# Optimization experiments

Hardware: AMD Instinct MI355X
Metric: run time of the kernel (lower is better)

The kernel has to match this reference:

```python
import jax, jax.numpy as jnp
from jax import lax
import numpy as np

DN = ('NCHW', 'OIHW', 'NCHW')


def conv3x3(x, w, b):
    y = lax.conv_general_dilated(x, w, (1, 1), ((1, 1), (1, 1)), dimension_numbers=DN)
    return y + b[None, :, None, None]


def box_mean(x, k):
    # Uniform k x k box mean with reflect padding; separable (exactly equal to
    # the dense ones/k^2 conv in the original since the kernel is rank-1).
    pad = k // 2
    C = x.shape[1]
    xp = jnp.pad(x, ((0, 0), (0, 0), (pad, pad), (pad, pad)), mode='reflect')
    kh = jnp.ones((C, 1, k, 1), x.dtype) / k
    kw = jnp.ones((C, 1, 1, k), x.dtype) / k
    y = lax.conv_general_dilated(xp, kh, (1, 1), 'VALID', feature_group_count=C, dimension_numbers=DN)
    y = lax.conv_general_dilated(y, kw, (1, 1), 'VALID', feature_group_count=C, dimension_numbers=DN)
    return y


def std_map_for_window(features, k):
    # features: [N, 8, H, W]
    C = features.shape[1]
    m = box_mean(features, k)
    m2 = box_mean(features * features, k)
    var = jnp.maximum(m2 - m * m, 1e-6)
    w = jax.nn.softmax(jnp.ones((C,), features.dtype))  # uniform (C==8 branch)
    sm = jnp.einsum('nchw,c->nhw', jnp.sqrt(var), w)[:, None]  # [N,1,H,W]
    return jnp.power(sm, 0.8)


def setup_inputs() -> dict:
    key = jax.random.key(0)
    ks = jax.random.split(key, 8)
    B, H, W = 8, 512, 512
    x = jax.random.normal(ks[0], (B, 4, H, W), dtype=jnp.float32)
    s = 0.05
    conv1_w = jax.random.normal(ks[1], (32, 4, 3, 3), jnp.float32) * s
    conv1_b = jnp.zeros((32,), jnp.float32)
    conv2_w = jax.random.normal(ks[2], (16, 32, 3, 3), jnp.float32) * s
    conv2_b = jnp.zeros((16,), jnp.float32)
    conv3_w = jax.random.normal(ks[3], (8, 16, 3, 3), jnp.float32) * s
    conv3_b = jnp.zeros((8,), jnp.float32)
    fusion_w = jnp.full((1, 3, 1, 1), 1.0 / 3.0, jnp.float32)  # init per module
    fusion_b = jnp.zeros((1,), jnp.float32)
    channel_weights = jnp.ones((4,), jnp.float32) / 4.0
    return dict(x=x, conv1_w=conv1_w, conv1_b=conv1_b, conv2_w=conv2_w,
                conv2_b=conv2_b, conv3_w=conv3_w, conv3_b=conv3_b,
                fusion_w=fusion_w, fusion_b=fusion_b,
                channel_weights=channel_weights)


def reference(x, conv1_w, conv1_b, conv2_w, conv2_b, conv3_w, conv3_b,
              fusion_w, fusion_b, channel_weights):
    window_sizes = (11, 25, 49)
    # feature extractor
    f = jax.nn.leaky_relu(conv3x3(x, conv1_w, conv1_b), 0.2)
    f = jax.nn.leaky_relu(conv3x3(f, conv2_w, conv2_b), 0.2)
    f = conv3x3(f, conv3_w, conv3_b)  # [B,8,H,W]
    # multi-scale std maps
    maps = [std_map_for_window(f, k) for k in window_sizes]
    multi = jnp.concatenate(maps, axis=1)  # [B,3,H,W]
    fused = jax.nn.relu(
        lax.conv_general_dilated(multi, fusion_w, (1, 1), 'VALID', dimension_numbers=DN)
        + fusion_b[None, :, None, None])  # [B,1,H,W]
    # adaptive thresholds
    std_flat = fused.ravel()
    q = jnp.quantile(std_flat, jnp.array([0.25, 0.75], fused.dtype))
    q25, q75 = q[0], q[1]
    iqr = q75 - q25
    iqr = jnp.where(iqr < 1e-5, jnp.asarray(0.05, fused.dtype), iqr)
    global_std = jnp.std(x, axis=(2, 3), keepdims=True, ddof=1)  # [B,4,1,1]
    lower = jnp.broadcast_to((q25 - 0.5 * iqr), global_std.shape)
    upper = jnp.broadcast_to((q75 + 0.5 * iqr), global_std.shape)
    gf = jnp.clip(global_std * 5.0, 0.5, 2.0)
    lower = lower * gf
    upper = upper * gf
    cw = jax.nn.softmax(channel_weights).reshape(1, 4, 1, 1)
    channel_std = jnp.std(x * cw, axis=(2, 3), keepdims=True, ddof=1)
    cf = jnp.clip(channel_std * 2.0, 0.8, 1.2)
    lower = lower * cf
    upper = upper * cf
    degenerate = jnp.min(jnp.abs(upper - lower)) < 1e-5
    mean_t = (upper + lower) / 2
    lower = jnp.where(degenerate, mean_t - 0.05, lower)
    upper = jnp.where(degenerate, mean_t + 0.05, upper)
    # texture mask
    diff = jnp.maximum(upper - lower, 1e-5)
    norm = jnp.clip((fused - lower) / diff, 0.0, 1.0)  # [B,4,H,W] via broadcast
    mask = jax.nn.sigmoid(6.0 * norm - 3.0)
    return jnp.mean(mask, axis=1, keepdims=True)  # [B,1,H,W]
```

## Files before the change

kernel.cpp:

```cpp
#include <hip/hip_runtime.h>
#include <hip/hip_bf16.h>
#include <math.h>


__global__ __launch_bounds__(256, 2) void conv12_k(
    const float* __restrict__ x,
    const float* __restrict__ w1,
    const float* __restrict__ b1,
    const float* __restrict__ w2,
    const float* __restrict__ b2,
    float* __restrict__ f2)
{
    __shared__ float xs[4 * 36 * 68];
    __shared__ float f1s[4 * 34 * 68];

    const int t  = threadIdx.x;
    const int tx = t & 7;
    const int ty = t >> 3;
    const int x0 = blockIdx.x * 64;
    const int y0 = blockIdx.y * 32;
    const int bb = blockIdx.z;
    const float* xb = x + (size_t)bb * 4 * 262144;

    for (int i = t; i < 9792; i += 256) {
        int ci  = i / 2448;
        int rem = i - ci * 2448;
        int r   = rem / 68;
        int c   = rem - r * 68;
        int Y = y0 - 2 + r, X = x0 - 2 + c;
        float v = 0.f;
        if ((unsigned)Y < 512u && (unsigned)X < 512u)
            v = xb[ci * 262144 + Y * 512 + X];
        xs[i] = v;
    }

    float acc[16][8];
#pragma unroll
    for (int j = 0; j < 16; ++j)
#pragma unroll
        for (int p = 0; p < 8; ++p) acc[j][p] = 0.f;

    for (int g = 0; g < 8; ++g) {
        __syncthreads();

#pragma unroll
        for (int fc = 0; fc < 4; ++fc) {
            const int foc = g * 4 + fc;
            float wv[36];
#pragma unroll
            for (int k = 0; k < 36; ++k) wv[k] = w1[foc * 36 + k];
            const float bias = b1[foc];
            for (int it = t; it < 578; it += 256) {
                int r  = it / 17;
                int q  = it - r * 17;
                int c0 = q * 4;
                int Y1 = y0 - 1 + r;
                float v[4] = {bias, bias, bias, bias};
#pragma unroll
                for (int ci = 0; ci < 4; ++ci) {
#pragma unroll
                    for (int ky = 0; ky < 3; ++ky) {
                        const float* xr = &xs[ci * 2448 + (r + ky) * 68 + c0];
                        float4 a  = *(const float4*)xr;
                        float2 bl = *(const float2*)(xr + 4);
                        float rr[6] = {a.x, a.y, a.z, a.w, bl.x, bl.y};
#pragma unroll
                        for (int kx = 0; kx < 3; ++kx) {
                            float w = wv[ci * 9 + ky * 3 + kx];
#pragma unroll
                            for (int p = 0; p < 4; ++p)
                                v[p] = fmaf(rr[p + kx], w, v[p]);
                        }
                    }
                }
                float st[4];
                bool rowok = ((unsigned)Y1 < 512u);
#pragma unroll
                for (int p = 0; p < 4; ++p) {
                    int X1 = x0 - 1 + c0 + p;
                    bool ok = rowok && ((unsigned)X1 < 512u) && (c0 + p <= 65);
                    float tv = v[p];
                    tv = tv > 0.f ? tv : 0.2f * tv;
                    st[p] = ok ? tv : 0.f;
                }
                *(float4*)&f1s[fc * 2312 + r * 68 + c0] =
                    make_float4(st[0], st[1], st[2], st[3]);
            }
        }
        __syncthreads();

#pragma unroll
        for (int fc = 0; fc < 4; ++fc) {
            const int ci = g * 4 + fc;
#pragma unroll
            for (int dy = 0; dy < 3; ++dy) {
                const float* rowp = &f1s[fc * 2312 + (ty + dy) * 68 + tx * 8];
                float4 a0 = *(const float4*)(rowp);
                float4 a1 = *(const float4*)(rowp + 4);
                float2 a2 = *(const float2*)(rowp + 8);
                float rr[10] = {a0.x, a0.y, a0.z, a0.w,
                                a1.x, a1.y, a1.z, a1.w, a2.x, a2.y};
#pragma unroll
                for (int j = 0; j < 16; ++j) {
#pragma unroll
                    for (int dx = 0; dx < 3; ++dx) {
                        float w = w2[(j * 32 + ci) * 9 + dy * 3 + dx];
#pragma unroll
                        for (int p = 0; p < 8; ++p)
                            acc[j][p] = fmaf(rr[p + dx], w, acc[j][p]);
                    }
                }
            }
        }
    }

    const int y = y0 + ty;
#pragma unroll
    for (int j = 0; j < 16; ++j) {
        float b = b2[j];
        float* op = f2 + (((size_t)bb * 16 + j) * 512 + y) * 512 + x0 + tx * 8;
        float v[8];
#pragma unroll
        for (int p = 0; p < 8; ++p) {
            float tv = acc[j][p] + b;
            v[p] = tv > 0.f ? tv : 0.2f * tv;
        }
        ((float4*)op)[0] = make_float4(v[0], v[1], v[2], v[3]);
        ((float4*)op)[1] = make_float4(v[4], v[5], v[6], v[7]);
    }
}

__global__ __launch_bounds__(256) void conv3_k(
    const float* __restrict__ in,
    const float* __restrict__ wgt,
    const float* __restrict__ bias,
    float* __restrict__ out)
{
    constexpr int TW = 64, TH = 32, SW = TW + 4;
    __shared__ float sl[(TH + 2) * SW];

    const int tx = threadIdx.x & 7;
    const int ty = threadIdx.x >> 3;
    const int x0 = blockIdx.x * TW;
    const int y0 = blockIdx.y * TH;
    const int bb = blockIdx.z;

    const float* inb = in + (size_t)bb * 16 * 262144;

    float acc[8][8];
#pragma unroll
    for (int j = 0; j < 8; ++j)
#pragma unroll
        for (int p = 0; p < 8; ++p) acc[j][p] = 0.f;

    for (int ci = 0; ci < 16; ++ci) {
        __syncthreads();
        const float* ip = inb + (size_t)ci * 262144;
        for (int idx = threadIdx.x; idx < (TH + 2) * (TW + 2); idx += 256) {
            int r  = idx / (TW + 2);
            int cc = idx - r * (TW + 2);
            int yy = y0 - 1 + r, xx = x0 - 1 + cc;
            float v = 0.f;
            if ((unsigned)yy < 512u && (unsigned)xx < 512u) v = ip[yy * 512 + xx];
            sl[r * SW + cc] = v;
        }
        __syncthreads();
        const float* wci = wgt + (size_t)ci * 9;
#pragma unroll
        for (int dy = 0; dy < 3; ++dy) {
            const float* rowp = &sl[(ty + dy) * SW + tx * 8];
            float4 a0 = *(const float4*)(rowp);
            float4 a1 = *(const float4*)(rowp + 4);
            float2 a2 = *(const float2*)(rowp + 8);
            float rr[10] = {a0.x, a0.y, a0.z, a0.w,
                            a1.x, a1.y, a1.z, a1.w, a2.x, a2.y};
#pragma unroll
            for (int j = 0; j < 8; ++j) {
#pragma unroll
                for (int dx = 0; dx < 3; ++dx) {
                    float w = wci[(size_t)j * 16 * 9 + dy * 3 + dx];
#pragma unroll
                    for (int p = 0; p < 8; ++p)
                        acc[j][p] = fmaf(rr[p + dx], w, acc[j][p]);
                }
            }
        }
    }

    const int y = y0 + ty;
#pragma unroll
    for (int j = 0; j < 8; ++j) {
        float b = bias[j];
        float* op = out + (((size_t)bb * 8 + j) * 512 + y) * 512 + x0 + tx * 8;
        float v[8];
#pragma unroll
        for (int p = 0; p < 8; ++p) v[p] = acc[j][p] + b;
        ((float4*)op)[0] = make_float4(v[0], v[1], v[2], v[3]);
        ((float4*)op)[1] = make_float4(v[4], v[5], v[6], v[7]);
    }
}

__device__ __forceinline__ float2 f2add(float2 a, float2 b) {
    return make_float2(a.x + b.x, a.y + b.y);
}
__device__ __forceinline__ int mir(int v) {
    return v < 0 ? -v : (v > 511 ? 1022 - v : v);
}

#define YB 4

__global__ __launch_bounds__(256) void stdmap_k(
    const float* __restrict__ f,
    const float* __restrict__ fw,
    const float* __restrict__ fbp,
    float* __restrict__ fused,
    int b0)
{
    const int total = gridDim.x * gridDim.y;
    const int lin   = blockIdx.y * gridDim.x + blockIdx.x;
    const int task  = (lin & 7) * (total >> 3) + (lin >> 3);
    const int bb    = task >> 7;
    const int y0    = (task & 127) * YB;
    const int t    = threadIdx.x;
    const int lane = t & 63, wid = t >> 6;

    __shared__ float S[3][2][513];
    __shared__ float wtt[4][6];

    const int   RAD[3] = {5, 12, 24};
    const float INV[3] = {1.f/121.f, 1.f/625.f, 1.f/2401.f};

    float smacc[3][YB][2];
#pragma unroll
    for (int sc = 0; sc < 3; ++sc)
#pragma unroll
        for (int yy = 0; yy < YB; ++yy)
            { smacc[sc][yy][0] = 0.f; smacc[sc][yy][1] = 0.f; }

    for (int c = 0; c < 8; ++c) {
        const float* base = f + ((size_t)bb * 8 + c) * 512 * 512;

        float2 wf[3], wq[3];
        {
            float2 sf[3] = {{0.f,0.f},{0.f,0.f},{0.f,0.f}};
            float2 sq[3] = {{0.f,0.f},{0.f,0.f},{0.f,0.f}};
#pragma unroll
            for (int dy = -24; dy <= 24; ++dy) {
                int row = mir(y0 + dy);
                float2 v  = ((const float2*)(base + (size_t)row * 512))[t];
                float2 vq = make_float2(v.x * v.x, v.y * v.y);
                int ad = dy < 0 ? -dy : dy;
                int ring = ad <= 5 ? 0 : (ad <= 12 ? 1 : 2);
                sf[ring] = f2add(sf[ring], v);
                sq[ring] = f2add(sq[ring], vq);
            }
            wf[0] = sf[0];               wq[0] = sq[0];
            wf[1] = f2add(sf[1], wf[0]); wq[1] = f2add(sq[1], wq[0]);
            wf[2] = f2add(sf[2], wf[1]); wq[2] = f2add(sq[2], wq[1]);
        }

        for (int yy = 0; yy < YB; ++yy) {
            const int y = y0 + yy;
            if (yy > 0) {
#pragma unroll
                for (int sc = 0; sc < 3; ++sc) {
                    int ra = mir(y + RAD[sc]);
                    int rs = mir(y - 1 - RAD[sc]);
                    float2 va = ((const float2*)(base + (size_t)ra * 512))[t];
                    float2 vs = ((const float2*)(base + (size_t)rs * 512))[t];
                    wf[sc].x += va.x - vs.x;       wf[sc].y += va.y - vs.y;
                    wq[sc].x += va.x*va.x - vs.x*vs.x;
                    wq[sc].y += va.y*va.y - vs.y*vs.y;
                }
            }

            float pf[3], pq[3], incf[3], incq[3];
#pragma unroll
            for (int sc = 0; sc < 3; ++sc) {
                pf[sc] = wf[sc].x + wf[sc].y;
                pq[sc] = wq[sc].x + wq[sc].y;
                incf[sc] = pf[sc]; incq[sc] = pq[sc];
            }
#pragma unroll
            for (int off = 1; off < 64; off <<= 1) {
#pragma unroll
                for (int sc = 0; sc < 3; ++sc) {
                    float uf = __shfl_up(incf[sc], (unsigned)off, 64);
                    float uq = __shfl_up(incq[sc], (unsigned)off, 64);
                    if (lane >= off) { incf[sc] += uf; incq[sc] += uq; }
                }
            }
            if (lane == 63) {
#pragma unroll
                for (int sc = 0; sc < 3; ++sc) {
                    wtt[wid][sc]     = incf[sc];
                    wtt[wid][3 + sc] = incq[sc];
                }
            }
            __syncthreads();
            float wpf[3] = {0.f,0.f,0.f}, wpq[3] = {0.f,0.f,0.f};
#pragma unroll
            for (int w = 0; w < 4; ++w)
                if (w < wid)
#pragma unroll
                    for (int sc = 0; sc < 3; ++sc) {
                        wpf[sc] += wtt[w][sc];
                        wpq[sc] += wtt[w][3 + sc];
                    }
#pragma unroll
            for (int sc = 0; sc < 3; ++sc) {
                float exf = wpf[sc] + incf[sc] - pf[sc];
                float exq = wpq[sc] + incq[sc] - pq[sc];
                S[sc][0][2*t+1] = exf + wf[sc].x;
                S[sc][0][2*t+2] = exf + pf[sc];
                S[sc][1][2*t+1] = exq + wq[sc].x;
                S[sc][1][2*t+2] = exq + pq[sc];
            }
            if (t == 0)
#pragma unroll
                for (int sc = 0; sc < 3; ++sc)
                    { S[sc][0][0] = 0.f; S[sc][1][0] = 0.f; }
            __syncthreads();

#pragma unroll
            for (int sc = 0; sc < 3; ++sc) {
                const int r = RAD[sc];
                const float* Sf = S[sc][0];
                const float* Sq = S[sc][1];
#pragma unroll
                for (int slot = 0; slot < 2; ++slot) {
                    int xx = 2*t + slot;
                    int lo = xx - r, hi = xx + r;
                    int loc = lo < 0 ? 0 : lo;
                    int hic = hi > 511 ? 511 : hi;
                    float wfv = Sf[hic + 1] - Sf[loc];
                    float wqv = Sq[hic + 1] - Sq[loc];
                    if (lo < 0)   { wfv += Sf[r - xx + 1] - Sf[1];
                                    wqv += Sq[r - xx + 1] - Sq[1]; }
                    if (hi > 511) { wfv += Sf[511] - Sf[1022 - xx - r];
                                    wqv += Sq[511] - Sq[1022 - xx - r]; }
                    float m   = wfv * INV[sc];
                    float m2  = wqv * INV[sc];
                    float var = m2 - m * m;
                    var = var > 1e-6f ? var : 1e-6f;
                    smacc[sc][yy][slot] += sqrtf(var);
                }
            }
            __syncthreads();
        }
    }

    const float w0 = fw[0], w1 = fw[1], w2 = fw[2], b = fbp[0];
#pragma unroll
    for (int yy = 0; yy < YB; ++yy) {
        float o[2];
#pragma unroll
        for (int slot = 0; slot < 2; ++slot) {
            float m0 = powf(smacc[0][yy][slot] * 0.125f, 0.8f);
            float m1 = powf(smacc[1][yy][slot] * 0.125f, 0.8f);
            float m2 = powf(smacc[2][yy][slot] * 0.125f, 0.8f);
            float fv = w0 * m0 + w1 * m1 + w2 * m2 + b;
            o[slot] = fv > 0.f ? fv : 0.f;
        }
        ((float2*)(fused + ((size_t)(b0 + bb) * 512 + y0 + yy) * 512))[t] =
            make_float2(o[0], o[1]);
    }
}

__global__ __launch_bounds__(256) void plane_std_part_k(
    const float* __restrict__ x, double* __restrict__ part)
{
    const int plane = blockIdx.x >> 5;
    const int blk   = blockIdx.x & 31;
    const float* p = x + (size_t)plane * 262144 + (size_t)blk * 8192;
    double s = 0.0, s2 = 0.0;
    for (int i = threadIdx.x; i < 2048; i += 256) {
        float4 v = ((const float4*)p)[i];
        s  += (double)v.x + (double)v.y + (double)v.z + (double)v.w;
        s2 += (double)v.x * v.x + (double)v.y * v.y
            + (double)v.z * v.z + (double)v.w * v.w;
    }
    __shared__ double ls[256], ls2[256];
    ls[threadIdx.x] = s; ls2[threadIdx.x] = s2;
    __syncthreads();
    for (int off = 128; off > 0; off >>= 1) {
        if (threadIdx.x < off) {
            ls[threadIdx.x]  += ls[threadIdx.x + off];
            ls2[threadIdx.x] += ls2[threadIdx.x + off];
        }
        __syncthreads();
    }
    if (threadIdx.x == 0) {
        part[2 * blockIdx.x]     = ls[0];
        part[2 * blockIdx.x + 1] = ls2[0];
    }
}

__global__ void plane_std_fin_k(const double* __restrict__ part,
                                float* __restrict__ stds)
{
    const int plane = threadIdx.x;
    if (plane >= 32) return;
    double s = 0.0, s2 = 0.0;
    for (int b = 0; b < 32; ++b) {
        s  += part[2 * (plane * 32 + b)];
        s2 += part[2 * (plane * 32 + b) + 1];
    }
    const double N = 262144.0;
    double var = (s2 - s * s / N) / (N - 1.0);
    stds[plane] = (float)sqrt(var > 0.0 ? var : 0.0);
}

__global__ __launch_bounds__(256) void hist1_k(
    const float* __restrict__ fused, unsigned* __restrict__ h)
{
    __shared__ unsigned lh[4096];
    for (int i = threadIdx.x; i < 4096; i += 256) lh[i] = 0u;
    __syncthreads();
    const int base = blockIdx.x * 2048;
    for (int i = threadIdx.x; i < 2048; i += 256) {
        unsigned bits = __float_as_uint(fused[base + i]);
        atomicAdd(&lh[bits >> 20], 1u);
    }
    __syncthreads();
    for (int i = threadIdx.x; i < 4096; i += 256) {
        unsigned c = lh[i];
        if (c) atomicAdd(&h[i], c);
    }
}

__global__ __launch_bounds__(256) void select_par_k(
    const unsigned* __restrict__ h, unsigned* __restrict__ pfx,
    unsigned* __restrict__ rem, int level)
{
    const int tt = blockIdx.x;
    const int t = threadIdx.x, lane = t & 63, wid = t >> 6;
    const unsigned targets[4] = {524287u, 524288u, 1572863u, 1572864u};
    const unsigned R = (level == 1) ? targets[tt] : rem[tt];
    const unsigned* hb = (level == 1) ? h : h + tt * 4096;

    unsigned loc[16], lsum = 0;
    const uint4* hv = (const uint4*)(hb + t * 16);
#pragma unroll
    for (int i = 0; i < 4; ++i) {
        uint4 v = hv[i];
        loc[4*i]=v.x; loc[4*i+1]=v.y; loc[4*i+2]=v.z; loc[4*i+3]=v.w;
        lsum += v.x + v.y + v.z + v.w;
    }
    __shared__ unsigned warr[4];
    __shared__ unsigned rbin, rrem;
    unsigned inc = lsum;
#pragma unroll
    for (int off = 1; off < 64; off <<= 1) {
        unsigned up = __shfl_up(inc, (unsigned)off, 64);
        if (lane >= off) inc += up;
    }
    if (lane == 63) warr[wid] = inc;
    __syncthreads();
    unsigned wpre = 0;
#pragma unroll
    for (int w = 0; w < 4; ++w) if (w < wid) wpre += warr[w];
    unsigned ex = wpre + inc - lsum;
    if (R >= ex && R < ex + lsum) {
        unsigned cum = ex;
#pragma unroll
        for (int i = 0; i < 16; ++i) {
            if (cum + loc[i] > R) { rbin = (unsigned)(t * 16 + i); rrem = R - cum; break; }
            cum += loc[i];
        }
    }
    __syncthreads();
    if (t == 0) {
        if (level == 1) { pfx[tt] = rbin << 20; rem[tt] = rrem; }
        else            { pfx[tt] |= rbin << 8; rem[tt] = rrem; }
    }
}

__global__ __launch_bounds__(256) void hist2_k(
    const float* __restrict__ fused, const unsigned* __restrict__ pfx,
    unsigned* __restrict__ h2)
{
    __shared__ unsigned lh[4 * 4096];
    for (int i = threadIdx.x; i < 4 * 4096; i += 256) lh[i] = 0u;
    unsigned p0 = pfx[0] >> 20, p1 = pfx[1] >> 20,
             p2 = pfx[2] >> 20, p3 = pfx[3] >> 20;
    __syncthreads();
    const int base = blockIdx.x * 2048;
    for (int i = threadIdx.x; i < 2048; i += 256) {
        unsigned bits = __float_as_uint(fused[base + i]);
        unsigned top = bits >> 20;
        unsigned mid = (bits >> 8) & 0xFFFu;
        if (top == p0) atomicAdd(&lh[0 * 4096 + mid], 1u);
        if (top == p1) atomicAdd(&lh[1 * 4096 + mid], 1u);
        if (top == p2) atomicAdd(&lh[2 * 4096 + mid], 1u);
        if (top == p3) atomicAdd(&lh[3 * 4096 + mid], 1u);
    }
    __syncthreads();
    for (int i = threadIdx.x; i < 4 * 4096; i += 256) {
        unsigned c = lh[i];
        if (c) atomicAdd(&h2[i], c);
    }
}

__global__ __launch_bounds__(256) void hist3_k(
    const float* __restrict__ fused, const unsigned* __restrict__ pfx,
    unsigned* __restrict__ h3)
{
    __shared__ unsigned lh[4 * 256];
    for (int i = threadIdx.x; i < 4 * 256; i += 256) lh[i] = 0u;
    unsigned p0 = pfx[0] >> 8, p1 = pfx[1] >> 8,
             p2 = pfx[2] >> 8, p3 = pfx[3] >> 8;
    __syncthreads();
    const int base = blockIdx.x * 2048;
    for (int i = threadIdx.x; i < 2048; i += 256) {
        unsigned bits = __float_as_uint(fused[base + i]);
        unsigned top = bits >> 8;
        unsigned low = bits & 0xFFu;
        if (top == p0) atomicAdd(&lh[0 * 256 + low], 1u);
        if (top == p1) atomicAdd(&lh[1 * 256 + low], 1u);
        if (top == p2) atomicAdd(&lh[2 * 256 + low], 1u);
        if (top == p3) atomicAdd(&lh[3 * 256 + low], 1u);
    }
    __syncthreads();
    for (int i = threadIdx.x; i < 4 * 256; i += 256) {
        unsigned c = lh[i];
        if (c) atomicAdd(&h3[i], c);
    }
}

__device__ __forceinline__ float clampf(float v, float lo, float hi) {
    return v < lo ? lo : (v > hi ? hi : v);
}

__global__ __launch_bounds__(256) void finalize_k(
    const unsigned* __restrict__ h3,
    const unsigned* __restrict__ pfx,
    const unsigned* __restrict__ rem,
    const float* __restrict__ stds,
    const float* __restrict__ cw,
    float* __restrict__ lu)
{
    const int tt = threadIdx.x >> 6, lane = threadIdx.x & 63;
    __shared__ float vals[4];

    {
        const unsigned R = rem[tt];
        const unsigned* h = h3 + tt * 256;
        uint4 v = ((const uint4*)h)[lane];
        unsigned loc[4] = {v.x, v.y, v.z, v.w};
        unsigned lsum = v.x + v.y + v.z + v.w;
        unsigned inc = lsum;
#pragma unroll
        for (int off = 1; off < 64; off <<= 1) {
            unsigned up = __shfl_up(inc, (unsigned)off, 64);
            if (lane >= off) inc += up;
        }
        unsigned ex = inc - lsum;
        if (R >= ex && R < ex + lsum) {
            unsigned cum = ex;
#pragma unroll
            for (int i = 0; i < 4; ++i) {
                if (cum + loc[i] > R) {
                    vals[tt] = __uint_as_float(pfx[tt] | (unsigned)(lane * 4 + i));
                    break;
                }
                cum += loc[i];
            }
        }
    }
    __syncthreads();
    if (threadIdx.x != 0) return;

    float q25 = vals[0] + 0.75f * (vals[1] - vals[0]);
    float q75 = vals[2] + 0.25f * (vals[3] - vals[2]);
    float iqr = q75 - q25;
    if (iqr < 1e-5f) iqr = 0.05f;
    float lo0 = q25 - 0.5f * iqr, up0 = q75 + 0.5f * iqr;

    float mx = cw[0];
    for (int c = 1; c < 4; ++c) mx = cw[c] > mx ? cw[c] : mx;
    float e[4], se = 0.f;
    for (int c = 0; c < 4; ++c) { e[c] = expf(cw[c] - mx); se += e[c]; }

    float l[32], u[32], mind = 1e30f;
    for (int p = 0; p < 32; ++p) {
        float sd = stds[p];
        int c = p & 3;
        float gf = clampf(sd * 5.f, 0.5f, 2.f);
        float cf = clampf(sd * (e[c] / se) * 2.f, 0.8f, 1.2f);
        l[p] = lo0 * gf * cf;
        u[p] = up0 * gf * cf;
        float d = fabsf(u[p] - l[p]);
        if (d < mind) mind = d;
    }
    bool deg = mind < 1e-5f;
    for (int p = 0; p < 32; ++p) {
        float L = l[p], U = u[p];
        if (deg) { float m = 0.5f * (L + U); L = m - 0.05f; U = m + 0.05f; }
        lu[p] = L; lu[32 + p] = U;
    }
}

__global__ __launch_bounds__(256) void mask_k(
    const float* __restrict__ fused, const float* __restrict__ lu,
    float* __restrict__ out)
{
    const int b = blockIdx.y;
    const int i = blockIdx.x * 256 + threadIdx.x;
    float fv = fused[(size_t)b * 262144 + i];
    float s = 0.f;
#pragma unroll
    for (int c = 0; c < 4; ++c) {
        float L = lu[b * 4 + c], U = lu[32 + b * 4 + c];
        float d = U - L; d = d > 1e-5f ? d : 1e-5f;
        float n = (fv - L) / d;
        n = n < 0.f ? 0.f : (n > 1.f ? 1.f : n);
        s += 1.f / (1.f + expf(3.f - 6.f * n));
    }
    out[(size_t)b * 262144 + i] = 0.25f * s;
}

extern "C" void kernel_launch(void* const* d_in, const int* in_sizes, int n_in,
                              void* d_out, int out_size, void* d_ws, size_t ws_size,
                              hipStream_t stream)
{
    const float* x   = (const float*)d_in[0];
    const float* c1w = (const float*)d_in[1];
    const float* c1b = (const float*)d_in[2];
    const float* c2w = (const float*)d_in[3];
    const float* c2b = (const float*)d_in[4];
    const float* c3w = (const float*)d_in[5];
    const float* c3b = (const float*)d_in[6];
    const float* fw  = (const float*)d_in[7];
    const float* fb  = (const float*)d_in[8];
    const float* cwt = (const float*)d_in[9];
    float* out = (float*)d_out;
    char* ws = (char*)d_ws;

    const size_t PLANE = 512 * 512;

    float* fused = (float*)ws;
    size_t off = 8 * PLANE * sizeof(float);
    float* stds = (float*)(ws + off); off += 32 * 4;
    float* lu   = (float*)(ws + off); off += 64 * 4;
    off = (off + 255) & ~(size_t)255;
    unsigned* pfx = (unsigned*)(ws + off); off += 16;
    unsigned* rem = (unsigned*)(ws + off); off += 16;
    off = (off + 255) & ~(size_t)255;
    unsigned* h1 = (unsigned*)(ws + off); off += 4096 * 4;
    unsigned* h2 = (unsigned*)(ws + off); off += 4 * 4096 * 4;
    unsigned* h3 = (unsigned*)(ws + off); off += 4 * 256 * 4;
    off = (off + 255) & ~(size_t)255;
    double* part = (double*)(ws + off); off += 1024 * 2 * sizeof(double);
    off = (off + 1023) & ~(size_t)1023;

    const size_t perb = 24 * PLANE * sizeof(float);
    int nb = 8;
    while (nb > 1 && off + (size_t)nb * perb > ws_size) nb >>= 1;
    float* f2  = (float*)(ws + off);
    float* fch = f2 + (size_t)nb * 16 * PLANE;

    hipLaunchKernelGGL(plane_std_part_k, dim3(1024), dim3(256), 0, stream, x, part);
    hipLaunchKernelGGL(plane_std_fin_k,  dim3(1),    dim3(64),  0, stream, part, stds);

    for (int b0 = 0; b0 < 8; b0 += nb) {
        const float* xc = x + (size_t)b0 * 4 * PLANE;
        hipLaunchKernelGGL(conv12_k, dim3(8, 16, nb), dim3(256), 0, stream,
                           xc, c1w, c1b, c2w, c2b, f2);
        hipLaunchKernelGGL(conv3_k,  dim3(8, 16, nb), dim3(256), 0, stream,
                           f2, c3w, c3b, fch);
        hipLaunchKernelGGL(stdmap_k, dim3(512 / YB, nb), dim3(256), 0, stream,
                           fch, fw, fb, fused, b0);
    }

    hipMemsetAsync(h1, 0, (4096 + 4 * 4096 + 4 * 256) * 4, stream);
    hipLaunchKernelGGL(hist1_k,     dim3(1024), dim3(256), 0, stream, fused, h1);
    hipLaunchKernelGGL(select_par_k, dim3(4),   dim3(256), 0, stream, h1, pfx, rem, 1);
    hipLaunchKernelGGL(hist2_k,     dim3(1024), dim3(256), 0, stream, fused, pfx, h2);
    hipLaunchKernelGGL(select_par_k, dim3(4),   dim3(256), 0, stream, h2, pfx, rem, 2);
    hipLaunchKernelGGL(hist3_k,     dim3(1024), dim3(256), 0, stream, fused, pfx, h3);
    hipLaunchKernelGGL(finalize_k,  dim3(1),    dim3(256), 0, stream,
                       h3, pfx, rem, stds, cwt, lu);
    hipLaunchKernelGGL(mask_k, dim3(1024, 8), dim3(256), 0, stream, fused, lu, out);
}
```

Baseline: 1.114 ms.

## Restructure fused conv1+conv2 kernel as row-streaming rolling buffer

```diff
diff --git a/kernel.cpp b/kernel.cpp
--- a/kernel.cpp
+++ b/kernel.cpp
@@ -3,7 +3,7 @@
 #include <math.h>
 
 
-__global__ __launch_bounds__(256, 2) void conv12_k(
+__global__ __launch_bounds__(256, 3) void conv12_k(
     const float* __restrict__ x,
     const float* __restrict__ w1,
     const float* __restrict__ b1,
@@ -11,122 +11,157 @@
     const float* __restrict__ b2,
     float* __restrict__ f2)
 {
-    __shared__ float xs[4 * 36 * 68];
-    __shared__ float f1s[4 * 34 * 68];
+    __shared__ float xr[3][4][68];
+    __shared__ float f1r[3][32][68];
+    __shared__ float w2s[32 * 16 * 12];
 
     const int t  = threadIdx.x;
-    const int tx = t & 7;
-    const int ty = t >> 3;
     const int x0 = blockIdx.x * 64;
     const int y0 = blockIdx.y * 32;
     const int bb = blockIdx.z;
     const float* xb = x + (size_t)bb * 4 * 262144;
 
-    for (int i = t; i < 9792; i += 256) {
-        int ci  = i / 2448;
-        int rem = i - ci * 2448;
-        int r   = rem / 68;
-        int c   = rem - r * 68;
-        int Y = y0 - 2 + r, X = x0 - 2 + c;
-        float v = 0.f;
-        if ((unsigned)Y < 512u && (unsigned)X < 512u)
-            v = xb[ci * 262144 + Y * 512 + X];
-        xs[i] = v;
-    }
-
-    float acc[16][8];
-#pragma unroll
-    for (int j = 0; j < 16; ++j)
-#pragma unroll
-        for (int p = 0; p < 8; ++p) acc[j][p] = 0.f;
-
-    for (int g = 0; g < 8; ++g) {
+    for (int i = t; i < 4608; i += 256) {
+        int kk = i % 9;
+        int r  = i / 9;
+        int j  = r & 15, ci = r >> 4;
+        w2s[(ci * 16 + j) * 12 + kk] = w2[(j * 32 + ci) * 9 + kk];
+    }
+
+    const int foc = t >> 3, oc = t & 7;
+    const int j2  = t >> 4, cg = t & 15;
+    float wv[36];
+#pragma unroll
+    for (int k = 0; k < 36; ++k) wv[k] = w1[foc * 36 + k];
+    const float f1b = b1[foc];
+    const float b2v = b2[j2];
+
+    auto stage_x = [&](int Y) {
+        const int slot = (unsigned)(Y + 516) % 3u;
+        for (int i = t; i < 272; i += 256) {
+            int ci = i / 68, c = i - ci * 68;
+            int X = x0 - 2 + c;
+            float v = 0.f;
+            if ((unsigned)Y < 512u && (unsigned)X < 512u)
+                v = xb[ci * 262144 + Y * 512 + X];
+            xr[slot][ci][c] = v;
+        }
+    };
+
+    auto f1_row = [&](int Y1) {
+        const int sw = (unsigned)(Y1 + 516) % 3u;
+        int sk[3];
+#pragma unroll
+        for (int ky = 0; ky < 3; ++ky) sk[ky] = (unsigned)(Y1 - 1 + ky + 516) % 3u;
+        const bool rowok = ((unsigned)Y1 < 512u);
+        const int C0 = oc * 8;
+        float v[8];
+#pragma unroll
+        for (int p = 0; p < 8; ++p) v[p] = f1b;
+#pragma unroll
+        for (int ci = 0; ci < 4; ++ci) {
+#pragma unroll
+            for (int ky = 0; ky < 3; ++ky) {
+                const float* xp = &xr[sk[ky]][ci][C0];
+                float4 A = *(const float4*)xp;
+                float4 B = *(const float4*)(xp + 4);
+                float2 Cq = *(const float2*)(xp + 8);
+                float rr[10] = {A.x,A.y,A.z,A.w,B.x,B.y,B.z,B.w,Cq.x,Cq.y};
+#pragma unroll
+                for (int kx = 0; kx < 3; ++kx) {
+                    float w = wv[ci * 9 + ky * 3 + kx];
+#pragma unroll
+                    for (int p = 0; p < 8; ++p)
+                        v[p] = fmaf(rr[p + kx], w, v[p]);
+                }
+            }
+        }
+        float st[8];
+#pragma unroll
+        for (int p = 0; p < 8; ++p) {
+            int X1 = x0 - 1 + C0 + p;
+            float tv = v[p]; tv = tv > 0.f ? tv : 0.2f * tv;
+            st[p] = (rowok && (unsigned)X1 < 512u) ? tv : 0.f;
+        }
+        *(float4*)&f1r[sw][foc][C0]     = make_float4(st[0],st[1],st[2],st[3]);
+        *(float4*)&f1r[sw][foc][C0 + 4] = make_float4(st[4],st[5],st[6],st[7]);
+        if (oc == 0) {
+            float u0 = f1b, u1 = f1b;
+#pragma unroll
+            for (int ci = 0; ci < 4; ++ci) {
+#pragma unroll
+                for (int ky = 0; ky < 3; ++ky) {
+                    const float* xp = &xr[sk[ky]][ci][64];
+                    float4 A = *(const float4*)xp;
+                    float rr[4] = {A.x, A.y, A.z, A.w};
+#pragma unroll
+                    for (int kx = 0; kx < 3; ++kx) {
+                        float w = wv[ci * 9 + ky * 3 + kx];
+                        u0 = fmaf(rr[kx],     w, u0);
+                        u1 = fmaf(rr[kx + 1], w, u1);
+                    }
+                }
+            }
+            u0 = u0 > 0.f ? u0 : 0.2f * u0;
+            u1 = u1 > 0.f ? u1 : 0.2f * u1;
+            int Xa = x0 + 63, Xb_ = x0 + 64;
+            float sa = (rowok && (unsigned)Xa  < 512u) ? u0 : 0.f;
+            float sb = (rowok && (unsigned)Xb_ < 512u) ? u1 : 0.f;
+            *(float4*)&f1r[sw][foc][64] = make_float4(sa, sb, 0.f, 0.f);
+        }
+    };
+
+    auto conv2_row = [&](int yo) {
+        int sd[3];
+#pragma unroll
+        for (int dy = 0; dy < 3; ++dy) sd[dy] = (unsigned)(yo - 1 + dy + 516) % 3u;
+        float a[4] = {0.f, 0.f, 0.f, 0.f};
+        for (int ci = 0; ci < 32; ++ci) {
+            const float* wp = &w2s[(ci * 16 + j2) * 12];
+            float4 W0 = *(const float4*)wp;
+            float4 W1 = *(const float4*)(wp + 4);
+            float  W8 = wp[8];
+            float wk[9] = {W0.x,W0.y,W0.z,W0.w,W1.x,W1.y,W1.z,W1.w,W8};
+#pragma unroll
+            for (int dy = 0; dy < 3; ++dy) {
+                const float* fp = &f1r[sd[dy]][ci][cg * 4];
+                float4 A = *(const float4*)fp;
+                float2 B = *(const float2*)(fp + 4);
+                float rr[6] = {A.x, A.y, A.z, A.w, B.x, B.y};
+#pragma unroll
+                for (int kx = 0; kx < 3; ++kx) {
+                    float w = wk[dy * 3 + kx];
+#pragma unroll
+                    for (int p = 0; p < 4; ++p)
+                        a[p] = fmaf(rr[p + kx], w, a[p]);
+                }
+            }
+        }
+        float o[4];
+#pragma unroll
+        for (int p = 0; p < 4; ++p) {
+            float tv = a[p] + b2v;
+            o[p] = tv > 0.f ? tv : 0.2f * tv;
+        }
+        *(float4*)(f2 + (((size_t)bb * 16 + j2) * 512 + yo) * 512 + x0 + cg * 4)
+            = make_float4(o[0], o[1], o[2], o[3]);
+    };
+
+    stage_x(y0 - 2); stage_x(y0 - 1); stage_x(y0);
+    __syncthreads();
+    f1_row(y0 - 1);
+    __syncthreads();
+    stage_x(y0 + 1);
+    __syncthreads();
+    f1_row(y0);
+    __syncthreads();
+
+    for (int yo = y0; yo < y0 + 32; ++yo) {
+        stage_x(yo + 2);
         __syncthreads();
-
-#pragma unroll
-        for (int fc = 0; fc < 4; ++fc) {
-            const int foc = g * 4 + fc;
-            float wv[36];
-#pragma unroll
-            for (int k = 0; k < 36; ++k) wv[k] = w1[foc * 36 + k];
-            const float bias = b1[foc];
-            for (int it = t; it < 578; it += 256) {
-                int r  = it / 17;
-                int q  = it - r * 17;
-                int c0 = q * 4;
-                int Y1 = y0 - 1 + r;
-                float v[4] = {bias, bias, bias, bias};
-#pragma unroll
-                for (int ci = 0; ci < 4; ++ci) {
-#pragma unroll
-                    for (int ky = 0; ky < 3; ++ky) {
-                        const float* xr = &xs[ci * 2448 + (r + ky) * 68 + c0];
-                        float4 a  = *(const float4*)xr;
-                        float2 bl = *(const float2*)(xr + 4);
-                        float rr[6] = {a.x, a.y, a.z, a.w, bl.x, bl.y};
-#pragma unroll
-                        for (int kx = 0; kx < 3; ++kx) {
-                            float w = wv[ci * 9 + ky * 3 + kx];
-#pragma unroll
-                            for (int p = 0; p < 4; ++p)
-                                v[p] = fmaf(rr[p + kx], w, v[p]);
-                        }
-                    }
-                }
-                float st[4];
-                bool rowok = ((unsigned)Y1 < 512u);
-#pragma unroll
-                for (int p = 0; p < 4; ++p) {
-                    int X1 = x0 - 1 + c0 + p;
-                    bool ok = rowok && ((unsigned)X1 < 512u) && (c0 + p <= 65);
-                    float tv = v[p];
-                    tv = tv > 0.f ? tv : 0.2f * tv;
-                    st[p] = ok ? tv : 0.f;
-                }
-                *(float4*)&f1s[fc * 2312 + r * 68 + c0] =
-                    make_float4(st[0], st[1], st[2], st[3]);
-            }
-        }
+        f1_row(yo + 1);
         __syncthreads();
-
-#pragma unroll
-        for (int fc = 0; fc < 4; ++fc) {
-            const int ci = g * 4 + fc;
-#pragma unroll
-            for (int dy = 0; dy < 3; ++dy) {
-                const float* rowp = &f1s[fc * 2312 + (ty + dy) * 68 + tx * 8];
-                float4 a0 = *(const float4*)(rowp);
-                float4 a1 = *(const float4*)(rowp + 4);
-                float2 a2 = *(const float2*)(rowp + 8);
-                float rr[10] = {a0.x, a0.y, a0.z, a0.w,
-                                a1.x, a1.y, a1.z, a1.w, a2.x, a2.y};
-#pragma unroll
-                for (int j = 0; j < 16; ++j) {
-#pragma unroll
-                    for (int dx = 0; dx < 3; ++dx) {
-                        float w = w2[(j * 32 + ci) * 9 + dy * 3 + dx];
-#pragma unroll
-                        for (int p = 0; p < 8; ++p)
-                            acc[j][p] = fmaf(rr[p + dx], w, acc[j][p]);
-                    }
-                }
-            }
-        }
-    }
-
-    const int y = y0 + ty;
-#pragma unroll
-    for (int j = 0; j < 16; ++j) {
-        float b = b2[j];
-        float* op = f2 + (((size_t)bb * 16 + j) * 512 + y) * 512 + x0 + tx * 8;
-        float v[8];
-#pragma unroll
-        for (int p = 0; p < 8; ++p) {
-            float tv = acc[j][p] + b;
-            v[p] = tv > 0.f ? tv : 0.2f * tv;
-        }
-        ((float4*)op)[0] = make_float4(v[0], v[1], v[2], v[3]);
-        ((float4*)op)[1] = make_float4(v[4], v[5], v[6], v[7]);
+        conv2_row(yo);
     }
 }
 
```

Result: slower. 1.404 ms (+26.0%).
